# Optimization experiments

Hardware: AMD Instinct MI355X
Metric: run time of the kernel (lower is better)

Reference implementation:

```python
import jax, jax.numpy as jnp
import numpy as np

D_MODEL = 4096
RANK = 16
BATCH = 4
SEQ = 4096


def setup_inputs() -> dict:
    key = jax.random.key(0)
    k_x, k_w, k_b, k_a, k_bb = jax.random.split(key, 5)
    x = jax.random.normal(k_x, (BATCH, SEQ, D_MODEL), dtype=jnp.float32)
    W = jax.random.normal(k_w, (D_MODEL, D_MODEL), dtype=jnp.float32) * 0.02
    bias = jax.random.normal(k_b, (D_MODEL,), dtype=jnp.float32) * 0.02
    A = jax.random.normal(k_a, (D_MODEL, RANK), dtype=jnp.float32) * 0.01
    B = jax.random.normal(k_bb, (RANK, D_MODEL), dtype=jnp.float32) * 0.01
    return {"x": x, "W": W, "bias": bias, "A": A, "B": B}


def reference(x, W, bias, A, B):
    # Faithful to the torch module: delta_W = A @ B; linear(x, W + delta_W, bias)
    # i.e. out = x @ (W + A @ B)^T + bias, with W: [d_out, d_in], x: [b, s, d_in].
    delta_W = A @ B                                   # [d_out, d_in]
    out = jnp.einsum("bsi,oi->bso", x, W + delta_W) + bias
    return out
```

## Files before the change

kernel.cpp:

```cpp
#include <hip/hip_runtime.h>
#include <stdint.h>


#define MDIM 16384
#define NDIM 4096
#define KDIM 4096
#define RANK 16
#define NT   (KDIM / 64)

typedef __bf16  bf16x8 __attribute__((ext_vector_type(8)));
typedef float   f32x4  __attribute__((ext_vector_type(4)));
typedef unsigned short u16x8 __attribute__((ext_vector_type(8)));

__device__ __forceinline__ unsigned short f2bf(float f) {
  union { float f; uint32_t u; } v; v.f = f;
  uint32_t r = v.u + 0x7FFFu + ((v.u >> 16) & 1u);
  return (unsigned short)(r >> 16);
}

__device__ __forceinline__ void gl16(const void* g, void* l) {
  __builtin_amdgcn_global_load_lds(
      (__attribute__((address_space(1))) void*)(g),
      (__attribute__((address_space(3))) void*)(l),
      16, 0, 0);
}

#define CAST_BLOCKS 32768
__global__ void prep_fused(const float* __restrict__ x,
                           const float* __restrict__ W,
                           const float* __restrict__ A,
                           const float* __restrict__ Bm,
                           unsigned short* __restrict__ xb,
                           unsigned short* __restrict__ Wp) {
  const int b = blockIdx.x;
  if (b < CAST_BLOCKS) {
    const size_t i = ((size_t)b * 256 + threadIdx.x) * 8;
    float4 a0 = *(const float4*)(x + i);
    float4 a1 = *(const float4*)(x + i + 4);
    u16x8 o;
    o[0] = f2bf(a0.x); o[1] = f2bf(a0.y); o[2] = f2bf(a0.z); o[3] = f2bf(a0.w);
    o[4] = f2bf(a1.x); o[5] = f2bf(a1.y); o[6] = f2bf(a1.z); o[7] = f2bf(a1.w);
    *(u16x8*)(xb + i) = o;
  } else {
    const size_t idx = ((size_t)(b - CAST_BLOCKS) * 256 + threadIdx.x) * 8;
    const int o  = (int)(idx >> 12);
    const int i0 = (int)(idx & 4095);
    float accv[8];
    {
      float4 w0 = *(const float4*)(W + (size_t)o * NDIM + i0);
      float4 w1 = *(const float4*)(W + (size_t)o * NDIM + i0 + 4);
      accv[0] = w0.x; accv[1] = w0.y; accv[2] = w0.z; accv[3] = w0.w;
      accv[4] = w1.x; accv[5] = w1.y; accv[6] = w1.z; accv[7] = w1.w;
    }
#pragma unroll
    for (int r = 0; r < RANK; ++r) {
      const float ar = A[o * RANK + r];
      float4 b0 = *(const float4*)(Bm + (size_t)r * NDIM + i0);
      float4 b1 = *(const float4*)(Bm + (size_t)r * NDIM + i0 + 4);
      accv[0] += ar * b0.x; accv[1] += ar * b0.y;
      accv[2] += ar * b0.z; accv[3] += ar * b0.w;
      accv[4] += ar * b1.x; accv[5] += ar * b1.y;
      accv[6] += ar * b1.z; accv[7] += ar * b1.w;
    }
    u16x8 ov;
#pragma unroll
    for (int j = 0; j < 8; ++j) ov[j] = f2bf(accv[j]);
    *(u16x8*)(Wp + idx) = ov;
  }
}

#define BARRIER  __builtin_amdgcn_s_barrier()
#define VMCNT8   asm volatile("s_waitcnt vmcnt(8)" ::: "memory")
#define VMCNT6   asm volatile("s_waitcnt vmcnt(6)" ::: "memory")
#define WAITVM0  asm volatile("s_waitcnt vmcnt(0)" ::: "memory")
#define LGKMC_(n) asm volatile("s_waitcnt lgkmcnt(" #n ")" ::: "memory")
#define LGKMC(n) LGKMC_(n)
#define SCHEDB   __builtin_amdgcn_sched_barrier(0)
#define PRIO1    __builtin_amdgcn_s_setprio(1)
#define PRIO0    __builtin_amdgcn_s_setprio(0)

#define DSR(dst, addr, imm)                                                   \
  asm volatile("ds_read_b128 %0, %1 offset:%c2"                               \
               : "=v"(dst) : "v"(addr), "n"(imm) : "memory")

#define STAGE_A(buf, h, kt) do {                                              \
    const int kc_ = ((kt) < NT ? (kt) : NT - 1);                              \
    const unsigned short* g_ = agb + (size_t)((h) * 64) * KDIM + kc_ * 64;    \
    unsigned short* d_ = &sA[(buf)][0] + (h) * 8192 + t * 8;                  \
    gl16(g_, d_);                                                             \
    gl16(g_ + (size_t)128 * KDIM, d_ + 4096);                                 \
  } while (0)

#define STAGE_B(buf, h, kt) do {                                              \
    const int kc_ = ((kt) < NT ? (kt) : NT - 1);                              \
    const unsigned short* g_ = bgb + (size_t)((h) * 32) * KDIM + kc_ * 64;    \
    unsigned short* d_ = &sB[(buf)][0] + (h) * 8192 + t * 8;                  \
    gl16(g_, d_);                                                             \
    gl16(g_ + (size_t)128 * KDIM, d_ + 4096);                                 \
  } while (0)

#define LDA(buf, mh) do {                                                     \
    DSR(a[0][0], aAddr0, (buf)*32768 + (mh)*16384 + 0);                       \
    DSR(a[0][1], aAddr1, (buf)*32768 + (mh)*16384 + 0);                       \
    DSR(a[1][0], aAddr0, (buf)*32768 + (mh)*16384 + 2048);                    \
    DSR(a[1][1], aAddr1, (buf)*32768 + (mh)*16384 + 2048);                    \
    DSR(a[2][0], aAddr0, (buf)*32768 + (mh)*16384 + 4096);                    \
    DSR(a[2][1], aAddr1, (buf)*32768 + (mh)*16384 + 4096);                    \
    DSR(a[3][0], aAddr0, (buf)*32768 + (mh)*16384 + 6144);                    \
    DSR(a[3][1], aAddr1, (buf)*32768 + (mh)*16384 + 6144);                    \
  } while (0)

#define LDB(bb, buf, nh) do {                                                 \
    DSR(bb[0][0], bAddr0, (buf)*32768 + (nh)*16384 + 0);                      \
    DSR(bb[0][1], bAddr1, (buf)*32768 + (nh)*16384 + 0);                      \
    DSR(bb[1][0], bAddr0, (buf)*32768 + (nh)*16384 + 2048);                   \
    DSR(bb[1][1], bAddr1, (buf)*32768 + (nh)*16384 + 2048);                   \
  } while (0)

#define MMmi(mh, nh, mi, bb) do {                                             \
    _Pragma("unroll") for (int ni = 0; ni < 2; ++ni)                          \
    _Pragma("unroll") for (int kk = 0; kk < 2; ++kk)                          \
      acc[(mh)*4+(mi)][(nh)*2+ni] = __builtin_amdgcn_mfma_f32_16x16x32_bf16(  \
          a[mi][kk], bb[ni][kk], acc[(mh)*4+(mi)][(nh)*2+ni], 0, 0, 0);       \
  } while (0)

#define MMni(mh, nh, ni, bb) do {                                             \
    _Pragma("unroll") for (int mi = 0; mi < 4; ++mi)                          \
    _Pragma("unroll") for (int kk = 0; kk < 2; ++kk)                          \
      acc[(mh)*4+mi][(nh)*2+(ni)] = __builtin_amdgcn_mfma_f32_16x16x32_bf16(  \
          a[mi][kk], bb[ni][kk], acc[(mh)*4+mi][(nh)*2+(ni)], 0, 0, 0);       \
  } while (0)

#define MMfull(mh, nh, bb) do {                                               \
    _Pragma("unroll") for (int mi = 0; mi < 4; ++mi)                          \
    _Pragma("unroll") for (int ni = 0; ni < 2; ++ni)                          \
    _Pragma("unroll") for (int kk = 0; kk < 2; ++kk)                          \
      acc[(mh)*4+mi][(nh)*2+ni] = __builtin_amdgcn_mfma_f32_16x16x32_bf16(    \
          a[mi][kk], bb[ni][kk], acc[(mh)*4+mi][(nh)*2+ni], 0, 0, 0);         \
  } while (0)

#define PH_A(bb, mh, nh)                                                      \
    PRIO1; LGKMC(6); SCHEDB; MMmi(mh, nh, 0, bb);                             \
    LGKMC(4); SCHEDB; MMmi(mh, nh, 1, bb);                                    \
    LGKMC(2); SCHEDB; MMmi(mh, nh, 2, bb);                                    \
    LGKMC(0); SCHEDB; MMmi(mh, nh, 3, bb); PRIO0

#define PH_B(bb, mh, nh)                                                      \
    PRIO1; LGKMC(2); SCHEDB; MMni(mh, nh, 0, bb);                             \
    LGKMC(0); SCHEDB; MMni(mh, nh, 1, bb); PRIO0

__global__ __launch_bounds__(512, 2) void gemm256(
    const unsigned short* __restrict__ Xb,
    const unsigned short* __restrict__ Wp,
    const float* __restrict__ bias,
    float* __restrict__ out) {
  __shared__ __align__(16) unsigned short sA[2][256 * 64];
  __shared__ __align__(16) unsigned short sB[2][256 * 64];

  const int t  = threadIdx.x;
  const int l  = t & 63;
  const int w  = t >> 6;
  const int wm = w >> 2;
  const int wn = w & 3;

  const int bid = blockIdx.x;
  const int swz = (bid & 7) * (1024 / 8) + (bid >> 3);
  const int bm  = (swz >> 4) * 256;
  const int bn  = (swz & 15) * 256;

  const int sr  = t >> 3;
  const int ske = (((t & 7) * 16) ^ ((sr & 7) << 4)) >> 1;
  const unsigned short* agb = Xb + (size_t)(bm + sr) * KDIM + ske;
  const unsigned short* bgb = Wp + (size_t)(bn + (sr >> 5) * 64 + (sr & 31)) * KDIM + ske;

  const int lr   = l & 15;
  const int koff = (l >> 4) * 8;
  const int xorE = (lr & 7) << 3;
  const unsigned ldsA = (unsigned)(uintptr_t)&sA[0][0];
  const unsigned ldsB = (unsigned)(uintptr_t)&sB[0][0];
  const unsigned aAddr0 = ldsA + (unsigned)((wm * 64 + lr) * 128 + ((koff ^ xorE) * 2));
  const unsigned aAddr1 = ldsA + (unsigned)((wm * 64 + lr) * 128 + (((32 + koff) ^ xorE) * 2));
  const unsigned bAddr0 = ldsB + (unsigned)((wn * 32 + lr) * 128 + ((koff ^ xorE) * 2));
  const unsigned bAddr1 = ldsB + (unsigned)((wn * 32 + lr) * 128 + (((32 + koff) ^ xorE) * 2));

  bf16x8 a[4][2], b0[2][2], b1[2][2];
  f32x4 acc[8][4];
#pragma unroll
  for (int i = 0; i < 8; ++i)
#pragma unroll
    for (int j = 0; j < 4; ++j)
      acc[i][j] = f32x4{0.f, 0.f, 0.f, 0.f};

  STAGE_A(0, 0, 0); STAGE_B(0, 0, 0); STAGE_A(0, 1, 0); STAGE_B(0, 1, 0);
  STAGE_A(1, 0, 1); STAGE_B(1, 0, 1); STAGE_B(1, 1, 1);
  VMCNT6;
  BARRIER;
  LDB(b0, 0, 0);

  for (int it = 0; it < NT / 2; ++it) {
    const int E = it * 2;
    LDA(0, 0);
    STAGE_A(1, 1, E + 1);
    BARRIER;
    PH_A(b0, 0, 0);
    VMCNT8;
    BARRIER;
    LDB(b1, 0, 1);
    STAGE_A(0, 0, E + 2);
    BARRIER;
    PH_B(b1, 0, 1);
    VMCNT8;
    BARRIER;
    LDA(0, 1);
    STAGE_B(0, 0, E + 2);
    BARRIER;
    PH_A(b1, 1, 1);
    VMCNT8;
    BARRIER;
    STAGE_B(0, 1, E + 2);
    BARRIER;
    PRIO1; MMfull(1, 0, b0); PRIO0;
    LDB(b0, 1, 0);
    VMCNT8;
    BARRIER;
    LDA(1, 0);
    STAGE_A(0, 1, E + 2);
    BARRIER;
    PH_A(b0, 0, 0);
    VMCNT8;
    BARRIER;
    LDB(b1, 1, 1);
    STAGE_A(1, 0, E + 3);
    BARRIER;
    PH_B(b1, 0, 1);
    VMCNT8;
    BARRIER;
    LDA(1, 1);
    STAGE_B(1, 0, E + 3);
    BARRIER;
    PH_A(b1, 1, 1);
    VMCNT8;
    BARRIER;
    STAGE_B(1, 1, E + 3);
    BARRIER;
    PRIO1; MMfull(1, 0, b0); PRIO0;
    LDB(b0, 0, 0);
    VMCNT8;
    BARRIER;
  }

  LGKMC(0);
  WAITVM0;

#pragma unroll
  for (int mf = 0; mf < 8; ++mf) {
#pragma unroll
    for (int nf = 0; nf < 4; ++nf) {
      const int row = bm + wm * 128 + mf * 16 + (l >> 4) * 4;
      const int col = bn + wn * 64 + nf * 16 + lr;
      const float bv = bias[col];
#pragma unroll
      for (int r = 0; r < 4; ++r)
        out[(size_t)(row + r) * NDIM + col] = acc[mf][nf][r] + bv;
    }
  }
}

extern "C" void kernel_launch(void* const* d_in, const int* in_sizes, int n_in,
                              void* d_out, int out_size, void* d_ws, size_t ws_size,
                              hipStream_t stream) {
  const float* x    = (const float*)d_in[0];
  const float* W    = (const float*)d_in[1];
  const float* bias = (const float*)d_in[2];
  const float* A    = (const float*)d_in[3];
  const float* B    = (const float*)d_in[4];
  float* out        = (float*)d_out;

  unsigned short* Wp = (unsigned short*)d_ws;
  unsigned short* Xb = (unsigned short*)d_ws + (size_t)NDIM * KDIM;

  prep_fused<<<dim3(CAST_BLOCKS + 8192), 256, 0, stream>>>(x, W, A, B, Xb, Wp);
  gemm256<<<dim3((MDIM / 256) * (NDIM / 256)), 512, 0, stream>>>(Xb, Wp, bias, out);
}
```

Before: 601.2 us.

## Restructure GEMM main loop schedule to halve barriers per phase

```diff
diff --git a/kernel.cpp b/kernel.cpp
--- a/kernel.cpp
+++ b/kernel.cpp
@@ -71,7 +71,6 @@
 
 #define BARRIER  __builtin_amdgcn_s_barrier()
 #define VMCNT8   asm volatile("s_waitcnt vmcnt(8)" ::: "memory")
-#define VMCNT6   asm volatile("s_waitcnt vmcnt(6)" ::: "memory")
 #define WAITVM0  asm volatile("s_waitcnt vmcnt(0)" ::: "memory")
 #define LGKMC_(n) asm volatile("s_waitcnt lgkmcnt(" #n ")" ::: "memory")
 #define LGKMC(n) LGKMC_(n)
@@ -191,62 +190,44 @@
     for (int j = 0; j < 4; ++j)
       acc[i][j] = f32x4{0.f, 0.f, 0.f, 0.f};
 
-  STAGE_A(0, 0, 0); STAGE_B(0, 0, 0); STAGE_A(0, 1, 0); STAGE_B(0, 1, 0);
-  STAGE_A(1, 0, 1); STAGE_B(1, 0, 1); STAGE_B(1, 1, 1);
-  VMCNT6;
+  STAGE_B(0, 0, 0); STAGE_A(0, 0, 0);
+  STAGE_B(0, 1, 0); STAGE_A(0, 1, 0);
+  STAGE_B(1, 0, 1); STAGE_A(1, 0, 1);
+  VMCNT8;
   BARRIER;
-  LDB(b0, 0, 0);
 
   for (int it = 0; it < NT / 2; ++it) {
     const int E = it * 2;
-    LDA(0, 0);
+    LDB(b0, 0, 0); LDA(0, 0);
+    STAGE_B(1, 1, E + 1);
+    VMCNT8; BARRIER;
+    PH_A(b0, 0, 0);
+    LDB(b1, 0, 1);
     STAGE_A(1, 1, E + 1);
-    BARRIER;
-    PH_A(b0, 0, 0);
-    VMCNT8;
-    BARRIER;
-    LDB(b1, 0, 1);
-    STAGE_A(0, 0, E + 2);
-    BARRIER;
+    VMCNT8; BARRIER;
     PH_B(b1, 0, 1);
-    VMCNT8;
-    BARRIER;
     LDA(0, 1);
     STAGE_B(0, 0, E + 2);
-    BARRIER;
+    VMCNT8; BARRIER;
     PH_A(b1, 1, 1);
-    VMCNT8;
-    BARRIER;
+    STAGE_A(0, 0, E + 2);
+    VMCNT8; BARRIER;
+    PRIO1; MMfull(1, 0, b0); PRIO0;
+    LDB(b0, 1, 0); LDA(1, 0);
     STAGE_B(0, 1, E + 2);
-    BARRIER;
-    PRIO1; MMfull(1, 0, b0); PRIO0;
-    LDB(b0, 1, 0);
-    VMCNT8;
-    BARRIER;
-    LDA(1, 0);
+    VMCNT8; BARRIER;
+    PH_A(b0, 0, 0);
+    LDB(b1, 1, 1);
     STAGE_A(0, 1, E + 2);
-    BARRIER;
-    PH_A(b0, 0, 0);
-    VMCNT8;
-    BARRIER;
-    LDB(b1, 1, 1);
-    STAGE_A(1, 0, E + 3);
-    BARRIER;
+    VMCNT8; BARRIER;
     PH_B(b1, 0, 1);
-    VMCNT8;
-    BARRIER;
     LDA(1, 1);
     STAGE_B(1, 0, E + 3);
-    BARRIER;
+    VMCNT8; BARRIER;
     PH_A(b1, 1, 1);
-    VMCNT8;
-    BARRIER;
-    STAGE_B(1, 1, E + 3);
-    BARRIER;
+    STAGE_A(1, 0, E + 3);
+    VMCNT8; BARRIER;
     PRIO1; MMfull(1, 0, b0); PRIO0;
-    LDB(b0, 0, 0);
-    VMCNT8;
-    BARRIER;
   }
 
   LGKMC(0);
```

Result: faster. 583.3 us, median of 2 (-3.0%).
